# Performance work log

Measured on AMD Instinct MI355X. Metric: run time of the kernel, lower is better.

The kernel has to match this reference:

```python
import jax, jax.numpy as jnp
import numpy as np

N_VAR = 100000
N_CON = 100000
N_EDGE = 2000000
C = 32  # all channel widths


def _linear(x, W, b):
    return x @ W.T + b


def setup_inputs() -> dict:
    key = jax.random.key(0)
    ks = jax.random.split(key, 16)
    s = 1.0 / np.sqrt(C)
    se = 1.0 / np.sqrt(3 * C)
    inp = {
        "var_f": jax.random.normal(ks[0], (N_VAR, C), jnp.float32),
        "con_f": jax.random.normal(ks[1], (N_CON, C), jnp.float32),
        "combined_edge_f": jax.random.normal(ks[2], (N_EDGE, C), jnp.float32),
        "edge_index_var_con": jax.random.randint(ks[3], (2, N_EDGE), 0, N_VAR, jnp.int32),
        # var_compress_mlp
        "Wv1": jax.random.uniform(ks[4], (C, C), jnp.float32, -s, s),
        "bv1": jnp.zeros((C,), jnp.float32),
        "Wv2": jax.random.uniform(ks[5], (C, C), jnp.float32, -s, s),
        "bv2": jnp.zeros((C,), jnp.float32),
        # con_compress_mlp
        "Wc1": jax.random.uniform(ks[6], (C, C), jnp.float32, -s, s),
        "bc1": jnp.zeros((C,), jnp.float32),
        "Wc2": jax.random.uniform(ks[7], (C, C), jnp.float32, -s, s),
        "bc2": jnp.zeros((C,), jnp.float32),
        # edge_mlp (input width = 3*C)
        "We1": jax.random.uniform(ks[8], (C, 3 * C), jnp.float32, -se, se),
        "be1": jnp.zeros((C,), jnp.float32),
        "We2": jax.random.uniform(ks[9], (C, C), jnp.float32, -s, s),
        "be2": jnp.zeros((C,), jnp.float32),
    }
    return inp


def reference(var_f, con_f, combined_edge_f, edge_index_var_con,
              Wv1, bv1, Wv2, bv2, Wc1, bc1, Wc2, bc2, We1, be1, We2, be2):
    # compress node features with 2-layer ReLU MLPs (done on nodes, not edges)
    v = jax.nn.relu(_linear(jax.nn.relu(_linear(var_f, Wv1, bv1)), Wv2, bv2))
    c = jax.nn.relu(_linear(jax.nn.relu(_linear(con_f, Wc1, bc1)), Wc2, bc2))
    # gather per-edge and concat: [E, 3C]
    out = jnp.concatenate(
        [combined_edge_f, v[edge_index_var_con[0]], c[edge_index_var_con[1]]], axis=1)
    # edge MLP: Linear -> ReLU -> Linear (no final ReLU)
    return _linear(jax.nn.relu(_linear(out, We1, be1)), We2, be2)
```

## Files before the change

kernel.cpp:

```cpp
#include <hip/hip_runtime.h>

typedef float  f32x2  __attribute__((ext_vector_type(2)));
typedef float  f32x4  __attribute__((ext_vector_type(4)));
typedef float  f32x16 __attribute__((ext_vector_type(16)));
typedef short  s16x4  __attribute__((ext_vector_type(4)));
typedef short  s16x8  __attribute__((ext_vector_type(8)));
typedef unsigned int u32x2 __attribute__((ext_vector_type(2)));

__device__ __forceinline__ unsigned f2bf(float f) {
    unsigned u = __builtin_bit_cast(unsigned, f);
    u += 0x7FFFu + ((u >> 16) & 1u);
    return u >> 16;
}
__device__ __forceinline__ s16x4 pack4(float a, float b, float c, float d) {
    u32x2 u;
    u[0] = f2bf(a) | (f2bf(b) << 16);
    u[1] = f2bf(c) | (f2bf(d) << 16);
    return __builtin_bit_cast(s16x4, u);
}
__device__ __forceinline__ s16x4 pack4v(f32x4 v) { return pack4(v[0], v[1], v[2], v[3]); }
__device__ __forceinline__ s16x4 lo4(s16x8 v) { return __builtin_shufflevector(v, v, 0, 1, 2, 3); }
__device__ __forceinline__ s16x4 hi4(s16x8 v) { return __builtin_shufflevector(v, v, 4, 5, 6, 7); }

__device__ __forceinline__ void node_body(
    const float* __restrict__ X,
    const float* __restrict__ W1, const float* __restrict__ b1,
    const float* __restrict__ W2, const float* __restrict__ b2,
    const float* __restrict__ Wm, const float* __restrict__ bm,
    unsigned short* __restrict__ outp, int N, int tile)
{
    const int lane = threadIdx.x & 63;
    const int g = lane >> 5, m = lane & 31;
    const int ntile = (N + 31) >> 5;
    if (tile >= ntile) return;

    s16x4 a1[4], a2[4], am[4];
#pragma unroll
    for (int q = 0; q < 4; ++q) {
        const float* p1 = W1 + m * 32 + 8 * q + 4 * g;
        a1[q] = pack4(p1[0], p1[1], p1[2], p1[3]);
        const float* p2 = W2 + m * 32 + 8 * q + 4 * g;
        a2[q] = pack4(p2[0], p2[1], p2[2], p2[3]);
        const float* pm = Wm + m * 96 + 8 * q + 4 * g;
        am[q] = pack4(pm[0], pm[1], pm[2], pm[3]);
    }
    f32x16 f1, f2, f3;
#pragma unroll
    for (int r = 0; r < 16; ++r) {
        int ch = (r & 3) + 8 * (r >> 2) + 4 * g;
        f1[r] = b1[ch];
        f2[r] = b2[ch];
        f3[r] = bm ? bm[ch] : 0.f;
    }

    const int node0 = tile * 32 + m;
    const int node = node0 < N ? node0 : N - 1;

    s16x4 bX[4];
#pragma unroll
    for (int q = 0; q < 4; ++q) {
        f32x4 v = *reinterpret_cast<const f32x4*>(X + (size_t)node * 32 + 8 * q + 4 * g);
        bX[q] = pack4v(v);
    }
    f32x16 acc = f1;
#pragma unroll
    for (int q = 0; q < 4; ++q) acc = __builtin_amdgcn_mfma_f32_32x32x8bf16_1k(a1[q], bX[q], acc, 0, 0, 0);
    s16x4 bH[4];
#pragma unroll
    for (int q = 0; q < 4; ++q)
        bH[q] = pack4(fmaxf(acc[4*q+0], 0.f), fmaxf(acc[4*q+1], 0.f),
                      fmaxf(acc[4*q+2], 0.f), fmaxf(acc[4*q+3], 0.f));
    acc = f2;
#pragma unroll
    for (int q = 0; q < 4; ++q) acc = __builtin_amdgcn_mfma_f32_32x32x8bf16_1k(a2[q], bH[q], acc, 0, 0, 0);
#pragma unroll
    for (int q = 0; q < 4; ++q)
        bH[q] = pack4(fmaxf(acc[4*q+0], 0.f), fmaxf(acc[4*q+1], 0.f),
                      fmaxf(acc[4*q+2], 0.f), fmaxf(acc[4*q+3], 0.f));
    acc = f3;
#pragma unroll
    for (int q = 0; q < 4; ++q) acc = __builtin_amdgcn_mfma_f32_32x32x8bf16_1k(am[q], bH[q], acc, 0, 0, 0);

    if (node0 < N) {
#pragma unroll
        for (int q = 0; q < 4; ++q) {
            s16x4 o = pack4(acc[4*q+0], acc[4*q+1], acc[4*q+2], acc[4*q+3]);
            *reinterpret_cast<s16x4*>(outp + (size_t)node0 * 32 + 8 * q + 4 * g) = o;
        }
    }
}

__global__ __launch_bounds__(256) void nodes_kernel(
    const float* __restrict__ var_f, const float* __restrict__ con_f,
    const float* __restrict__ Wv1, const float* __restrict__ bv1,
    const float* __restrict__ Wv2, const float* __restrict__ bv2,
    const float* __restrict__ Wc1, const float* __restrict__ bc1,
    const float* __restrict__ Wc2, const float* __restrict__ bc2,
    const float* __restrict__ We1, const float* __restrict__ be1,
    unsigned short* __restrict__ pv, unsigned short* __restrict__ pc,
    int nV, int nC, int blocksV)
{
    const int wv = threadIdx.x >> 6;
    if ((int)blockIdx.x < blocksV) {
        node_body(var_f, Wv1, bv1, Wv2, bv2, We1 + 32, be1, pv, nV, blockIdx.x * 4 + wv);
    } else {
        node_body(con_f, Wc1, bc1, Wc2, bc2, We1 + 64, nullptr, pc, nC,
                  (blockIdx.x - blocksV) * 4 + wv);
    }
}

__global__ __launch_bounds__(256, 4) void edge_kernel(
    const float* __restrict__ Ef, const int* __restrict__ idx,
    const unsigned short* __restrict__ pv, const unsigned short* __restrict__ pc,
    const float* __restrict__ We1, const float* __restrict__ We2,
    const float* __restrict__ be2,
    float* __restrict__ out, int nE)
{
    __shared__ float ldso[4 * 1088];
    const int lane = threadIdx.x & 63;
    const int wv = threadIdx.x >> 6;
    const int g = lane >> 5, n = lane & 31;
    float* ldsw = ldso + wv * 1088;

    s16x4 aW1[4], aI[4], aW2[4];
#pragma unroll
    for (int q = 0; q < 4; ++q) {
        const float* p = We1 + n * 96 + 16 * g + 4 * q;
        aW1[q] = pack4(p[0], p[1], p[2], p[3]);
        s16x4 r;
#pragma unroll
        for (int j = 0; j < 4; ++j) r[j] = (short)((16 * g + 4 * q + j == n) ? 0x3F80 : 0);
        aI[q] = r;
        const float* p2 = We2 + n * 32 + 8 * q + 4 * g;
        aW2[q] = pack4(p2[0], p2[1], p2[2], p2[3]);
    }
    s16x4 aB2 = {}, bOne = {};
    if (g == 0) {
        aB2[0] = (short)f2bf(be2[n]);
        bOne[0] = (short)0x3F80;
    }

    const int ntile = nE >> 5;
    const int nw = (gridDim.x * blockDim.x) >> 6;
    int t = (blockIdx.x * blockDim.x + threadIdx.x) >> 6;
    if (t >= ntile) return;

    int e = t * 32 + n;
    int i0c = __builtin_nontemporal_load(idx + e);
    int i1c = __builtin_nontemporal_load(idx + nE + e);
    const float* efp = Ef + (size_t)e * 32 + 16 * g;
    f32x4 ef0 = __builtin_nontemporal_load(reinterpret_cast<const f32x4*>(efp + 0));
    f32x4 ef1 = __builtin_nontemporal_load(reinterpret_cast<const f32x4*>(efp + 4));
    f32x4 ef2 = __builtin_nontemporal_load(reinterpret_cast<const f32x4*>(efp + 8));
    f32x4 ef3 = __builtin_nontemporal_load(reinterpret_cast<const f32x4*>(efp + 12));

    while (true) {
        const int tn = t + nw;
        const int tc = tn < ntile ? tn : t;

        const unsigned short* pvr = pv + (size_t)i0c * 32 + 16 * g;
        const unsigned short* pcr = pc + (size_t)i1c * 32 + 16 * g;
        s16x8 gv0 = *reinterpret_cast<const s16x8*>(pvr);
        s16x8 gv1 = *reinterpret_cast<const s16x8*>(pvr + 8);
        s16x8 gc0 = *reinterpret_cast<const s16x8*>(pcr);
        s16x8 gc1 = *reinterpret_cast<const s16x8*>(pcr + 8);

        const int en = tc * 32 + n;
        int i0n = __builtin_nontemporal_load(idx + en);
        int i1n = __builtin_nontemporal_load(idx + nE + en);
        const float* efpn = Ef + (size_t)en * 32 + 16 * g;
        f32x4 efn0 = __builtin_nontemporal_load(reinterpret_cast<const f32x4*>(efpn + 0));
        f32x4 efn1 = __builtin_nontemporal_load(reinterpret_cast<const f32x4*>(efpn + 4));
        f32x4 efn2 = __builtin_nontemporal_load(reinterpret_cast<const f32x4*>(efpn + 8));
        f32x4 efn3 = __builtin_nontemporal_load(reinterpret_cast<const f32x4*>(efpn + 12));

        f32x16 acc = {};
        {
            s16x4 bE0 = pack4v(ef0), bE1 = pack4v(ef1), bE2 = pack4v(ef2), bE3 = pack4v(ef3);
            acc = __builtin_amdgcn_mfma_f32_32x32x8bf16_1k(aW1[0], bE0, acc, 0, 0, 0);
            acc = __builtin_amdgcn_mfma_f32_32x32x8bf16_1k(aW1[1], bE1, acc, 0, 0, 0);
            acc = __builtin_amdgcn_mfma_f32_32x32x8bf16_1k(aW1[2], bE2, acc, 0, 0, 0);
            acc = __builtin_amdgcn_mfma_f32_32x32x8bf16_1k(aW1[3], bE3, acc, 0, 0, 0);
        }
        acc = __builtin_amdgcn_mfma_f32_32x32x8bf16_1k(aI[0], lo4(gv0), acc, 0, 0, 0);
        acc = __builtin_amdgcn_mfma_f32_32x32x8bf16_1k(aI[1], hi4(gv0), acc, 0, 0, 0);
        acc = __builtin_amdgcn_mfma_f32_32x32x8bf16_1k(aI[2], lo4(gv1), acc, 0, 0, 0);
        acc = __builtin_amdgcn_mfma_f32_32x32x8bf16_1k(aI[3], hi4(gv1), acc, 0, 0, 0);
        acc = __builtin_amdgcn_mfma_f32_32x32x8bf16_1k(aI[0], lo4(gc0), acc, 0, 0, 0);
        acc = __builtin_amdgcn_mfma_f32_32x32x8bf16_1k(aI[1], hi4(gc0), acc, 0, 0, 0);
        acc = __builtin_amdgcn_mfma_f32_32x32x8bf16_1k(aI[2], lo4(gc1), acc, 0, 0, 0);
        acc = __builtin_amdgcn_mfma_f32_32x32x8bf16_1k(aI[3], hi4(gc1), acc, 0, 0, 0);

        s16x4 bH[4];
#pragma unroll
        for (int q = 0; q < 4; ++q)
            bH[q] = pack4(fmaxf(acc[4*q+0], 0.f), fmaxf(acc[4*q+1], 0.f),
                          fmaxf(acc[4*q+2], 0.f), fmaxf(acc[4*q+3], 0.f));

        f32x16 acc2 = {};
        acc2 = __builtin_amdgcn_mfma_f32_32x32x8bf16_1k(aB2, bOne, acc2, 0, 0, 0);
#pragma unroll
        for (int q = 0; q < 4; ++q)
            acc2 = __builtin_amdgcn_mfma_f32_32x32x8bf16_1k(aW2[q], bH[q], acc2, 0, 0, 0);

        {
            float* orow = ldsw + n * 34;
#pragma unroll
            for (int q = 0; q < 4; ++q) {
                f32x2 lo; lo[0] = acc2[4*q+0]; lo[1] = acc2[4*q+1];
                f32x2 hi; hi[0] = acc2[4*q+2]; hi[1] = acc2[4*q+3];
                *reinterpret_cast<f32x2*>(orow + 8 * q + 4 * g)     = lo;
                *reinterpret_cast<f32x2*>(orow + 8 * q + 4 * g + 2) = hi;
            }
            float* obase = out + (size_t)t * 1024;
#pragma unroll
            for (int p = 0; p < 4; ++p) {
                int li = p * 256 + lane * 4;
                int row = li >> 5, col = li & 31;
                const float* s = ldsw + row * 34 + col;
                f32x2 lo = *reinterpret_cast<const f32x2*>(s);
                f32x2 hi = *reinterpret_cast<const f32x2*>(s + 2);
                f32x4 v; v[0] = lo[0]; v[1] = lo[1]; v[2] = hi[0]; v[3] = hi[1];
                __builtin_nontemporal_store(v, reinterpret_cast<f32x4*>(obase + li));
            }
        }

        if (tn >= ntile) break;
        t = tn;
        i0c = i0n; i1c = i1n;
        ef0 = efn0; ef1 = efn1; ef2 = efn2; ef3 = efn3;
    }
}

extern "C" void kernel_launch(void* const* d_in, const int* in_sizes, int n_in,
                              void* d_out, int out_size, void* d_ws, size_t ws_size,
                              hipStream_t stream) {
    const float* var_f = (const float*)d_in[0];
    const float* con_f = (const float*)d_in[1];
    const float* Ef    = (const float*)d_in[2];
    const int*   idx   = (const int*)d_in[3];
    const float* Wv1 = (const float*)d_in[4];
    const float* bv1 = (const float*)d_in[5];
    const float* Wv2 = (const float*)d_in[6];
    const float* bv2 = (const float*)d_in[7];
    const float* Wc1 = (const float*)d_in[8];
    const float* bc1 = (const float*)d_in[9];
    const float* Wc2 = (const float*)d_in[10];
    const float* bc2 = (const float*)d_in[11];
    const float* We1 = (const float*)d_in[12];
    const float* be1 = (const float*)d_in[13];
    const float* We2 = (const float*)d_in[14];
    const float* be2 = (const float*)d_in[15];
    float* out = (float*)d_out;

    const int nV = in_sizes[0] / 32;
    const int nC = in_sizes[1] / 32;
    const int nE = in_sizes[2] / 32;

    unsigned short* pv = (unsigned short*)d_ws;
    unsigned short* pc = pv + (size_t)nV * 32;

    const int blocksV = ((((nV + 31) >> 5) + 3) / 4);
    const int blocksC = ((((nC + 31) >> 5) + 3) / 4);
    nodes_kernel<<<blocksV + blocksC, 256, 0, stream>>>(
        var_f, con_f, Wv1, bv1, Wv2, bv2, Wc1, bc1, Wc2, bc2,
        We1, be1, pv, pc, nV, nC, blocksV);

    edge_kernel<<<1024, 256, 0, stream>>>(Ef, idx, pv, pc, We1, We2, be2, out, nE);
}
```

Before: 195.9 us.

## Store node projections in fp32 and add them directly instead of identity MFMAs

The precomputed per-node projections are now written as fp32 instead of bf16. The edge kernel adds the gathered var and con contributions straight into the accumulator, replacing eight identity-matrix MFMAs per tile. This removes matrix-core work, but doubles the bytes gathered per edge from the node tables. Other changes: each node wave now processes four tiles, the edge kernel's cross-iteration prefetch of edge features is dropped in favor of loading in the current iteration, and occupancy goes to 6 blocks with a 1536-block grid.

Result: slower. 210.6 us (+7.5%).

```diff
diff --git a/kernel.cpp b/kernel.cpp
--- a/kernel.cpp
+++ b/kernel.cpp
@@ -4,7 +4,6 @@
 typedef float  f32x4  __attribute__((ext_vector_type(4)));
 typedef float  f32x16 __attribute__((ext_vector_type(16)));
 typedef short  s16x4  __attribute__((ext_vector_type(4)));
-typedef short  s16x8  __attribute__((ext_vector_type(8)));
 typedef unsigned int u32x2 __attribute__((ext_vector_type(2)));
 
 __device__ __forceinline__ unsigned f2bf(float f) {
@@ -19,20 +18,18 @@
     return __builtin_bit_cast(s16x4, u);
 }
 __device__ __forceinline__ s16x4 pack4v(f32x4 v) { return pack4(v[0], v[1], v[2], v[3]); }
-__device__ __forceinline__ s16x4 lo4(s16x8 v) { return __builtin_shufflevector(v, v, 0, 1, 2, 3); }
-__device__ __forceinline__ s16x4 hi4(s16x8 v) { return __builtin_shufflevector(v, v, 4, 5, 6, 7); }
 
 __device__ __forceinline__ void node_body(
     const float* __restrict__ X,
     const float* __restrict__ W1, const float* __restrict__ b1,
     const float* __restrict__ W2, const float* __restrict__ b2,
     const float* __restrict__ Wm, const float* __restrict__ bm,
-    unsigned short* __restrict__ outp, int N, int tile)
+    float* __restrict__ outp, int N, int tile0)
 {
     const int lane = threadIdx.x & 63;
     const int g = lane >> 5, m = lane & 31;
     const int ntile = (N + 31) >> 5;
-    if (tile >= ntile) return;
+    if (tile0 >= ntile) return;
 
     s16x4 a1[4], a2[4], am[4];
 #pragma unroll
@@ -53,39 +50,46 @@
         f3[r] = bm ? bm[ch] : 0.f;
     }
 
-    const int node0 = tile * 32 + m;
-    const int node = node0 < N ? node0 : N - 1;
-
-    s16x4 bX[4];
-#pragma unroll
-    for (int q = 0; q < 4; ++q) {
-        f32x4 v = *reinterpret_cast<const f32x4*>(X + (size_t)node * 32 + 8 * q + 4 * g);
-        bX[q] = pack4v(v);
-    }
-    f32x16 acc = f1;
-#pragma unroll
-    for (int q = 0; q < 4; ++q) acc = __builtin_amdgcn_mfma_f32_32x32x8bf16_1k(a1[q], bX[q], acc, 0, 0, 0);
-    s16x4 bH[4];
-#pragma unroll
-    for (int q = 0; q < 4; ++q)
-        bH[q] = pack4(fmaxf(acc[4*q+0], 0.f), fmaxf(acc[4*q+1], 0.f),
-                      fmaxf(acc[4*q+2], 0.f), fmaxf(acc[4*q+3], 0.f));
-    acc = f2;
-#pragma unroll
-    for (int q = 0; q < 4; ++q) acc = __builtin_amdgcn_mfma_f32_32x32x8bf16_1k(a2[q], bH[q], acc, 0, 0, 0);
-#pragma unroll
-    for (int q = 0; q < 4; ++q)
-        bH[q] = pack4(fmaxf(acc[4*q+0], 0.f), fmaxf(acc[4*q+1], 0.f),
-                      fmaxf(acc[4*q+2], 0.f), fmaxf(acc[4*q+3], 0.f));
-    acc = f3;
-#pragma unroll
-    for (int q = 0; q < 4; ++q) acc = __builtin_amdgcn_mfma_f32_32x32x8bf16_1k(am[q], bH[q], acc, 0, 0, 0);
-
-    if (node0 < N) {
+#pragma unroll
+    for (int k = 0; k < 4; ++k) {
+        const int tile = tile0 + k;
+        if (tile >= ntile) break;
+        const int node0 = tile * 32 + m;
+        const int node = node0 < N ? node0 : N - 1;
+
+        s16x4 bX[4];
 #pragma unroll
         for (int q = 0; q < 4; ++q) {
-            s16x4 o = pack4(acc[4*q+0], acc[4*q+1], acc[4*q+2], acc[4*q+3]);
-            *reinterpret_cast<s16x4*>(outp + (size_t)node0 * 32 + 8 * q + 4 * g) = o;
+            f32x4 v = *reinterpret_cast<const f32x4*>(X + (size_t)node * 32 + 8 * q + 4 * g);
+            bX[q] = pack4v(v);
+        }
+        f32x16 acc = f1;
+#pragma unroll
+        for (int q = 0; q < 4; ++q) acc = __builtin_amdgcn_mfma_f32_32x32x8bf16_1k(a1[q], bX[q], acc, 0, 0, 0);
+        s16x4 bH[4];
+#pragma unroll
+        for (int q = 0; q < 4; ++q)
+            bH[q] = pack4(fmaxf(acc[4*q+0], 0.f), fmaxf(acc[4*q+1], 0.f),
+                          fmaxf(acc[4*q+2], 0.f), fmaxf(acc[4*q+3], 0.f));
+        acc = f2;
+#pragma unroll
+        for (int q = 0; q < 4; ++q) acc = __builtin_amdgcn_mfma_f32_32x32x8bf16_1k(a2[q], bH[q], acc, 0, 0, 0);
+#pragma unroll
+        for (int q = 0; q < 4; ++q)
+            bH[q] = pack4(fmaxf(acc[4*q+0], 0.f), fmaxf(acc[4*q+1], 0.f),
+                          fmaxf(acc[4*q+2], 0.f), fmaxf(acc[4*q+3], 0.f));
+        acc = f3;
+#pragma unroll
+        for (int q = 0; q < 4; ++q) acc = __builtin_amdgcn_mfma_f32_32x32x8bf16_1k(am[q], bH[q], acc, 0, 0, 0);
+
+        if (node0 < N) {
+            float* orow = outp + (size_t)node0 * 32 + 16 * g;
+#pragma unroll
+            for (int q = 0; q < 4; ++q) {
+                f32x4 v; v[0] = acc[4*q+0]; v[1] = acc[4*q+1];
+                v[2] = acc[4*q+2]; v[3] = acc[4*q+3];
+                *reinterpret_cast<f32x4*>(orow + 4 * q) = v;
+            }
         }
     }
 }
@@ -97,21 +101,21 @@
     const float* __restrict__ Wc1, const float* __restrict__ bc1,
     const float* __restrict__ Wc2, const float* __restrict__ bc2,
     const float* __restrict__ We1, const float* __restrict__ be1,
-    unsigned short* __restrict__ pv, unsigned short* __restrict__ pc,
-    int nV, int nC, int blocksV)
+    float* __restrict__ pv, float* __restrict__ pc,
+    int nV, int nC, int wavesV)
 {
-    const int wv = threadIdx.x >> 6;
-    if ((int)blockIdx.x < blocksV) {
-        node_body(var_f, Wv1, bv1, Wv2, bv2, We1 + 32, be1, pv, nV, blockIdx.x * 4 + wv);
+    const int wvg = (blockIdx.x * blockDim.x + threadIdx.x) >> 6;
+    if (wvg < wavesV) {
+        node_body(var_f, Wv1, bv1, Wv2, bv2, We1 + 32, be1, pv, nV, wvg * 4);
     } else {
         node_body(con_f, Wc1, bc1, Wc2, bc2, We1 + 64, nullptr, pc, nC,
-                  (blockIdx.x - blocksV) * 4 + wv);
-    }
-}
-
-__global__ __launch_bounds__(256, 4) void edge_kernel(
+                  (wvg - wavesV) * 4);
+    }
+}
+
+__global__ __launch_bounds__(256, 6) void edge_kernel(
     const float* __restrict__ Ef, const int* __restrict__ idx,
-    const unsigned short* __restrict__ pv, const unsigned short* __restrict__ pc,
+    const float* __restrict__ pv, const float* __restrict__ pc,
     const float* __restrict__ We1, const float* __restrict__ We2,
     const float* __restrict__ be2,
     float* __restrict__ out, int nE)
@@ -122,15 +126,11 @@
     const int g = lane >> 5, n = lane & 31;
     float* ldsw = ldso + wv * 1088;
 
-    s16x4 aW1[4], aI[4], aW2[4];
+    s16x4 aW1[4], aW2[4];
 #pragma unroll
     for (int q = 0; q < 4; ++q) {
         const float* p = We1 + n * 96 + 16 * g + 4 * q;
         aW1[q] = pack4(p[0], p[1], p[2], p[3]);
-        s16x4 r;
-#pragma unroll
-        for (int j = 0; j < 4; ++j) r[j] = (short)((16 * g + 4 * q + j == n) ? 0x3F80 : 0);
-        aI[q] = r;
         const float* p2 = We2 + n * 32 + 8 * q + 4 * g;
         aW2[q] = pack4(p2[0], p2[1], p2[2], p2[3]);
     }
@@ -145,34 +145,31 @@
     int t = (blockIdx.x * blockDim.x + threadIdx.x) >> 6;
     if (t >= ntile) return;
 
-    int e = t * 32 + n;
-    int i0c = __builtin_nontemporal_load(idx + e);
-    int i1c = __builtin_nontemporal_load(idx + nE + e);
-    const float* efp = Ef + (size_t)e * 32 + 16 * g;
-    f32x4 ef0 = __builtin_nontemporal_load(reinterpret_cast<const f32x4*>(efp + 0));
-    f32x4 ef1 = __builtin_nontemporal_load(reinterpret_cast<const f32x4*>(efp + 4));
-    f32x4 ef2 = __builtin_nontemporal_load(reinterpret_cast<const f32x4*>(efp + 8));
-    f32x4 ef3 = __builtin_nontemporal_load(reinterpret_cast<const f32x4*>(efp + 12));
+    int e0 = t * 32 + n;
+    int i0 = idx[e0], i1 = idx[nE + e0];
 
     while (true) {
         const int tn = t + nw;
+
+        const float* efp = Ef + (size_t)(t * 32 + n) * 32 + 16 * g;
+        f32x4 ef0 = *reinterpret_cast<const f32x4*>(efp + 0);
+        f32x4 ef1 = *reinterpret_cast<const f32x4*>(efp + 4);
+        f32x4 ef2 = *reinterpret_cast<const f32x4*>(efp + 8);
+        f32x4 ef3 = *reinterpret_cast<const f32x4*>(efp + 12);
+        const float* pvr = pv + (size_t)i0 * 32 + 16 * g;
+        const float* pcr = pc + (size_t)i1 * 32 + 16 * g;
+        f32x4 gv0 = *reinterpret_cast<const f32x4*>(pvr + 0);
+        f32x4 gv1 = *reinterpret_cast<const f32x4*>(pvr + 4);
+        f32x4 gv2 = *reinterpret_cast<const f32x4*>(pvr + 8);
+        f32x4 gv3 = *reinterpret_cast<const f32x4*>(pvr + 12);
+        f32x4 gc0 = *reinterpret_cast<const f32x4*>(pcr + 0);
+        f32x4 gc1 = *reinterpret_cast<const f32x4*>(pcr + 4);
+        f32x4 gc2 = *reinterpret_cast<const f32x4*>(pcr + 8);
+        f32x4 gc3 = *reinterpret_cast<const f32x4*>(pcr + 12);
         const int tc = tn < ntile ? tn : t;
-
-        const unsigned short* pvr = pv + (size_t)i0c * 32 + 16 * g;
-        const unsigned short* pcr = pc + (size_t)i1c * 32 + 16 * g;
-        s16x8 gv0 = *reinterpret_cast<const s16x8*>(pvr);
-        s16x8 gv1 = *reinterpret_cast<const s16x8*>(pvr + 8);
-        s16x8 gc0 = *reinterpret_cast<const s16x8*>(pcr);
-        s16x8 gc1 = *reinterpret_cast<const s16x8*>(pcr + 8);
-
         const int en = tc * 32 + n;
-        int i0n = __builtin_nontemporal_load(idx + en);
-        int i1n = __builtin_nontemporal_load(idx + nE + en);
-        const float* efpn = Ef + (size_t)en * 32 + 16 * g;
-        f32x4 efn0 = __builtin_nontemporal_load(reinterpret_cast<const f32x4*>(efpn + 0));
-        f32x4 efn1 = __builtin_nontemporal_load(reinterpret_cast<const f32x4*>(efpn + 4));
-        f32x4 efn2 = __builtin_nontemporal_load(reinterpret_cast<const f32x4*>(efpn + 8));
-        f32x4 efn3 = __builtin_nontemporal_load(reinterpret_cast<const f32x4*>(efpn + 12));
+        const int i0n = idx[en];
+        const int i1n = idx[nE + en];
 
         f32x16 acc = {};
         {
@@ -182,14 +179,13 @@
             acc = __builtin_amdgcn_mfma_f32_32x32x8bf16_1k(aW1[2], bE2, acc, 0, 0, 0);
             acc = __builtin_amdgcn_mfma_f32_32x32x8bf16_1k(aW1[3], bE3, acc, 0, 0, 0);
         }
-        acc = __builtin_amdgcn_mfma_f32_32x32x8bf16_1k(aI[0], lo4(gv0), acc, 0, 0, 0);
-        acc = __builtin_amdgcn_mfma_f32_32x32x8bf16_1k(aI[1], hi4(gv0), acc, 0, 0, 0);
-        acc = __builtin_amdgcn_mfma_f32_32x32x8bf16_1k(aI[2], lo4(gv1), acc, 0, 0, 0);
-        acc = __builtin_amdgcn_mfma_f32_32x32x8bf16_1k(aI[3], hi4(gv1), acc, 0, 0, 0);
-        acc = __builtin_amdgcn_mfma_f32_32x32x8bf16_1k(aI[0], lo4(gc0), acc, 0, 0, 0);
-        acc = __builtin_amdgcn_mfma_f32_32x32x8bf16_1k(aI[1], hi4(gc0), acc, 0, 0, 0);
-        acc = __builtin_amdgcn_mfma_f32_32x32x8bf16_1k(aI[2], lo4(gc1), acc, 0, 0, 0);
-        acc = __builtin_amdgcn_mfma_f32_32x32x8bf16_1k(aI[3], hi4(gc1), acc, 0, 0, 0);
+        {
+            f32x4 s0 = gv0 + gc0, s1 = gv1 + gc1, s2 = gv2 + gc2, s3 = gv3 + gc3;
+            acc[0]  += s0[0]; acc[1]  += s0[1]; acc[2]  += s0[2]; acc[3]  += s0[3];
+            acc[4]  += s1[0]; acc[5]  += s1[1]; acc[6]  += s1[2]; acc[7]  += s1[3];
+            acc[8]  += s2[0]; acc[9]  += s2[1]; acc[10] += s2[2]; acc[11] += s2[3];
+            acc[12] += s3[0]; acc[13] += s3[1]; acc[14] += s3[2]; acc[15] += s3[3];
+        }
 
         s16x4 bH[4];
 #pragma unroll
@@ -226,9 +222,7 @@
         }
 
         if (tn >= ntile) break;
-        t = tn;
-        i0c = i0n; i1c = i1n;
-        ef0 = efn0; ef1 = efn1; ef2 = efn2; ef3 = efn3;
+        t = tn; i0 = i0n; i1 = i1n;
     }
 }
 
@@ -257,14 +251,15 @@
     const int nC = in_sizes[1] / 32;
     const int nE = in_sizes[2] / 32;
 
-    unsigned short* pv = (unsigned short*)d_ws;
-    unsigned short* pc = pv + (size_t)nV * 32;
-
-    const int blocksV = ((((nV + 31) >> 5) + 3) / 4);
-    const int blocksC = ((((nC + 31) >> 5) + 3) / 4);
-    nodes_kernel<<<blocksV + blocksC, 256, 0, stream>>>(
+    float* pv = (float*)d_ws;
+    float* pc = pv + (size_t)nV * 32;
+
+    const int wavesV = (((nV + 31) >> 5) + 3) >> 2;
+    const int wavesC = (((nC + 31) >> 5) + 3) >> 2;
+    const int nodeBlocks = (wavesV + wavesC + 3) / 4;
+    nodes_kernel<<<nodeBlocks, 256, 0, stream>>>(
         var_f, con_f, Wv1, bv1, Wv2, bv2, Wc1, bc1, Wc2, bc2,
-        We1, be1, pv, pc, nV, nC, blocksV);
-
-    edge_kernel<<<1024, 256, 0, stream>>>(Ef, idx, pv, pc, We1, We2, be2, out, nE);
-}
+        We1, be1, pv, pc, nV, nC, wavesV);
+
+    edge_kernel<<<1536, 256, 0, stream>>>(Ef, idx, pv, pc, We1, We2, be2, out, nE);
+}
```
